# Kernel optimization log

Measured on AMD Instinct MI355X. Metric: run time of the kernel, lower is better.

The kernel has to match this reference:

```python
import jax, jax.numpy as jnp
import numpy as np

N = 50000          # nodes
E = 1_600_000      # edges
IN = 256           # in_channels
C = 32             # hidden_channels (per-head width)
HEADS = 4
BN_EPS = 1e-5


def setup_inputs() -> dict:
    key = jax.random.key(0)
    ks = jax.random.split(key, 32)
    g = lambda k, shp, s=0.1: (jax.random.normal(k, shp, jnp.float32) * s)
    inp = {
        "x": jax.random.normal(ks[0], (N, IN), jnp.float32),
        "edge_index": jax.random.randint(ks[1], (2, E), 0, N, jnp.int64),
        "edge_attr": jax.random.uniform(ks[2], (E, 1), jnp.float32),
        # conv1 (GATConv in=IN, out=C, heads=HEADS, edge_dim=1)
        "W1": g(ks[3], (IN, HEADS * C)),
        "as1": g(ks[4], (HEADS, C)),
        "ad1": g(ks[5], (HEADS, C)),
        "We1": g(ks[6], (1, HEADS * C)),
        "ae1": g(ks[7], (HEADS, C)),
        "b1": jnp.zeros((HEADS * C,), jnp.float32),
        # bn1 (eval mode, running_mean=0, running_var=1)
        "g1": jnp.ones((HEADS * C,), jnp.float32),
        "be1": jnp.zeros((HEADS * C,), jnp.float32),
        # conv2 (GATConv in=HEADS*C, out=C, heads=1, concat=False, edge_dim=1)
        "W2": g(ks[8], (HEADS * C, C)),
        "as2": g(ks[9], (1, C)),
        "ad2": g(ks[10], (1, C)),
        "We2": g(ks[11], (1, C)),
        "ae2": g(ks[12], (1, C)),
        "b2": jnp.zeros((C,), jnp.float32),
        # bn2
        "g2": jnp.ones((C,), jnp.float32),
        "be2": jnp.zeros((C,), jnp.float32),
        # classifier: Linear(C,16) -> ReLU -> Linear(16,2)
        "Wc1": g(ks[13], (C, 16)),
        "bc1": jnp.zeros((16,), jnp.float32),
        "Wc2": g(ks[14], (16, 2)),
        "bc2": jnp.zeros((2,), jnp.float32),
        "Wr1": g(ks[15], (C, 16)),
        "br1": jnp.zeros((16,), jnp.float32),
        "Wr2": g(ks[16], (16, 1)),
        "br2": jnp.zeros((1,), jnp.float32),
    }
    return inp


def _gat_conv(x, src, dst, eattr, W, a_src, a_dst, We, a_e, bias, heads, c, concat):
    n = x.shape[0]
    xs = (x @ W).reshape(n, heads, c)                       # [N,H,C]
    al_s = (xs * a_src).sum(-1)                              # [N,H]
    al_d = (xs * a_dst).sum(-1)                              # [N,H]
    ee = (eattr @ We).reshape(-1, heads, c)                  # [E,H,C]
    al_e = (ee * a_e).sum(-1)                                # [E,H]
    alpha = al_s[src] + al_d[dst] + al_e                     # [E,H]
    alpha = jax.nn.leaky_relu(alpha, 0.2)
    # segment softmax over destination node
    mx = jax.ops.segment_max(alpha, dst, num_segments=n)
    ex = jnp.exp(alpha - mx[dst])
    den = jax.ops.segment_sum(ex, dst, num_segments=n)
    a = ex / (den[dst] + 1e-16)                              # [E,H]
    out = jax.ops.segment_sum(xs[src] * a[..., None], dst, num_segments=n)  # [N,H,C]
    out = out.reshape(n, heads * c) if concat else out.mean(axis=1)
    return out + bias


def _add_self_loops(src, dst, eattr, n):
    loop = jnp.arange(n, dtype=src.dtype)
    fill = jnp.broadcast_to(eattr.mean(axis=0, keepdims=True), (n, eattr.shape[1]))
    return (jnp.concatenate([src, loop]), jnp.concatenate([dst, loop]),
            jnp.concatenate([eattr, fill], axis=0))


def _bn_eval(x, gamma, beta):
    # running_mean=0, running_var=1 (fresh BatchNorm1d, eval mode)
    return x * (gamma / jnp.sqrt(1.0 + BN_EPS)) + beta


def reference(x, edge_index, edge_attr, W1, as1, ad1, We1, ae1, b1, g1, be1,
              W2, as2, ad2, We2, ae2, b2, g2, be2,
              Wc1, bc1, Wc2, bc2, Wr1, br1, Wr2, br2):
    n = x.shape[0]
    src, dst, ea = _add_self_loops(edge_index[0], edge_index[1], edge_attr, n)
    h = _gat_conv(x, src, dst, ea, W1, as1, ad1, We1, ae1, b1, HEADS, C, True)
    h = jax.nn.elu(_bn_eval(h, g1, be1))
    h = _gat_conv(h, src, dst, ea, W2, as2, ad2, We2, ae2, b2, 1, C, False)
    h = jax.nn.elu(_bn_eval(h, g2, be2))
    cls = jax.nn.relu(h @ Wc1 + bc1) @ Wc2 + bc2             # [N,2]
    reg = (jax.nn.relu(h @ Wr1 + br1) @ Wr2 + br2)[:, 0]     # [N]
    return cls, reg, h
```

## Files before the change

kernel.cpp:

```cpp
#include <hip/hip_runtime.h>
#include <cstdint>
#include <cstddef>

#define NN 50000
#define EE 1600000
#define IN_DIM 256
#define HC 128
#define CD 32
#define BN_RS 0.9999950000374997f

#define CAP1 128
#define CAP2 128
#define NBKT 196
#define S1_B 782
#define HIST_B 160
#define G1_B 782

typedef __attribute__((ext_vector_type(8))) short short8;
typedef __attribute__((ext_vector_type(4))) float f32x4;

__device__ __forceinline__ float lrelu(float a) { return a > 0.f ? a : 0.2f * a; }
__device__ __forceinline__ float elu(float a) { return a > 0.f ? a : (__expf(a) - 1.f); }

__device__ __forceinline__ unsigned short f2bf(float f) {
    unsigned int u = __float_as_uint(f);
    unsigned int r = (u + 0x7FFFu + ((u >> 16) & 1u)) >> 16;
    return (unsigned short)r;
}
__device__ __forceinline__ float bf2f(unsigned short b) {
    return __uint_as_float(((unsigned int)b) << 16);
}
__device__ __forceinline__ float2 bf2f2(unsigned int p) {
    float2 r;
    r.x = __uint_as_float(p << 16);
    r.y = __uint_as_float(p & 0xFFFF0000u);
    return r;
}
__device__ __forceinline__ void unpack_edge(unsigned long long p, int& s, float& eav) {
    s = (int)(unsigned int)(p & 0xFFFFFFFFull);
    eav = __uint_as_float((unsigned int)(p >> 32));
}

__device__ __forceinline__ int block_excl_scan_256(int v, int tid, int* wsum) {
    int lane = tid & 63, wv = tid >> 6;
    int x = v;
    #pragma unroll
    for (int off = 1; off < 64; off <<= 1) {
        int y = __shfl_up(x, off);
        if (lane >= off) x += y;
    }
    if (lane == 63) wsum[wv] = x;
    __syncthreads();
    int wpre = 0;
    #pragma unroll
    for (int w = 0; w < 4; w++)
        if (w < wv) wpre += wsum[w];
    return wpre + x - v;
}

__global__ __launch_bounds__(256) void k0_prep(const float* __restrict__ W1,
                                               const float* __restrict__ W2,
                                               const float* __restrict__ We1,
                                               const float* __restrict__ ae1,
                                               const float* __restrict__ We2,
                                               const float* __restrict__ ae2,
                                               unsigned short* __restrict__ W1hi,
                                               unsigned short* __restrict__ W1lo,
                                               unsigned short* __restrict__ W2hi,
                                               unsigned short* __restrict__ W2lo,
                                               float* __restrict__ consts) {
    int blk = blockIdx.x;
    int tid = threadIdx.x;
    if (blk < 16) {
        int t = blk * 256 + tid;
        int lane = t & 63;
        int kt = (t >> 6) & 7;
        int nt = t >> 9;
        int kbase = kt * 32 + (lane >> 4) * 8;
        int col = nt * 16 + (lane & 15);
        size_t obase = (size_t)t * 8;
        #pragma unroll
        for (int j = 0; j < 8; j++) {
            float w = W1[(size_t)(kbase + j) * HC + col];
            unsigned short h = f2bf(w);
            W1hi[obase + j] = h;
            W1lo[obase + j] = f2bf(w - bf2f(h));
        }
    } else if (blk < 18) {
        int t = (blk - 16) * 256 + tid;
        int lane = t & 63;
        int kt = (t >> 6) & 3;
        int nt = t >> 8;
        int kbase = kt * 32 + (lane >> 4) * 8;
        int col = nt * 16 + (lane & 15);
        size_t obase = (size_t)t * 8;
        #pragma unroll
        for (int j = 0; j < 8; j++) {
            float w = W2[(size_t)(kbase + j) * CD + col];
            unsigned short h = f2bf(w);
            W2hi[obase + j] = h;
            W2lo[obase + j] = f2bf(w - bf2f(h));
        }
    } else {
        if (tid < 4) {
            float s = 0.f;
            for (int c = 0; c < 32; c++) s += We1[tid * 32 + c] * ae1[tid * 32 + c];
            consts[2 + tid] = s;
        } else if (tid == 4) {
            float s = 0.f;
            for (int c = 0; c < 32; c++) s += We2[c] * ae2[c];
            consts[6] = s;
        }
    }
}

__global__ __launch_bounds__(256) void kA_hist_gemm1(const int* __restrict__ ei,
                                                     const float* __restrict__ ea,
                                                     const float* __restrict__ x,
                                                     const unsigned short* __restrict__ Whi,
                                                     const unsigned short* __restrict__ Wlo,
                                                     int* __restrict__ bucketHist,
                                                     float* __restrict__ easum,
                                                     unsigned short* __restrict__ xs1b) {
    __shared__ int h[256];
    int tid = threadIdx.x;
    if (blockIdx.x < HIST_B) {
        h[tid] = 0;
        __syncthreads();
        float s = 0.f;
        for (int i = blockIdx.x * 256 + tid; i < EE; i += HIST_B * 256) {
            atomicAdd(&h[ei[EE + i] >> 8], 1);
            s += ea[i];
        }
        __syncthreads();
        if (tid < NBKT && h[tid] > 0) atomicAdd(&bucketHist[tid], h[tid]);
        #pragma unroll
        for (int off = 32; off > 0; off >>= 1) s += __shfl_xor(s, off);
        if ((tid & 63) == 0) atomicAdd(easum, s);
    } else {
        int lane = tid & 63, wv = tid >> 6;
        int row0 = (blockIdx.x - HIST_B) * 64 + wv * 16;
        if (row0 >= NN) return;
        int m = lane & 15;
        int q = lane >> 4;
        f32x4 acc[8];
        #pragma unroll
        for (int nt = 0; nt < 8; nt++) acc[nt] = {0.f, 0.f, 0.f, 0.f};
        const float* xrow = x + (size_t)(row0 + m) * IN_DIM + q * 8;
        #pragma unroll
        for (int kt = 0; kt < 8; kt++) {
            float4 v0 = *(const float4*)(xrow + kt * 32);
            float4 v1 = *(const float4*)(xrow + kt * 32 + 4);
            float vv[8] = {v0.x, v0.y, v0.z, v0.w, v1.x, v1.y, v1.z, v1.w};
            short8 ahi, alo;
            #pragma unroll
            for (int j = 0; j < 8; j++) {
                unsigned short hh = f2bf(vv[j]);
                ahi[j] = (short)hh;
                alo[j] = (short)f2bf(vv[j] - bf2f(hh));
            }
            #pragma unroll
            for (int nt = 0; nt < 8; nt++) {
                size_t fb = ((size_t)(nt * 8 + kt) * 64 + lane) * 8;
                short8 bhi = *(const short8*)(Whi + fb);
                short8 blo = *(const short8*)(Wlo + fb);
                acc[nt] = __builtin_amdgcn_mfma_f32_16x16x32_bf16(ahi, bhi, acc[nt], 0, 0, 0);
                acc[nt] = __builtin_amdgcn_mfma_f32_16x16x32_bf16(ahi, blo, acc[nt], 0, 0, 0);
                acc[nt] = __builtin_amdgcn_mfma_f32_16x16x32_bf16(alo, bhi, acc[nt], 0, 0, 0);
            }
        }
        #pragma unroll
        for (int nt = 0; nt < 8; nt++) {
            #pragma unroll
            for (int reg = 0; reg < 4; reg++) {
                int row = row0 + q * 4 + reg;
                xs1b[(size_t)row * HC + nt * 16 + m] = f2bf(acc[nt][reg]);
            }
        }
    }
}

__global__ void bucket_scan(const int* __restrict__ bucketHist,
                            int* __restrict__ bucketBase,
                            int* __restrict__ bucketCursor,
                            int* __restrict__ indptr,
                            float* __restrict__ consts) {
    __shared__ int wsum[4];
    int tid = threadIdx.x;
    int v = (tid < NBKT) ? bucketHist[tid] : 0;
    int excl = block_excl_scan_256(v, tid, wsum);
    if (tid <= NBKT) bucketBase[tid] = (tid == NBKT) ? EE : excl;
    if (tid < NBKT) bucketCursor[tid] = excl;
    if (tid == 0) { indptr[NN] = EE; consts[1] = consts[0] / (float)EE; }
}

__global__ __launch_bounds__(256) void kB_stage1_al1(const int* __restrict__ ei,
                                                     const float* __restrict__ ea,
                                                     int* __restrict__ bucketCursor,
                                                     int* __restrict__ Adst,
                                                     int* __restrict__ Asrc,
                                                     float* __restrict__ Aea,
                                                     const unsigned short* __restrict__ xs1b,
                                                     const float* __restrict__ as1,
                                                     const float* __restrict__ ad1,
                                                     float* __restrict__ als,
                                                     float* __restrict__ ald) {
    __shared__ int cnt[256];
    __shared__ int basel[256];
    __shared__ int gbase[256];
    __shared__ int wsum[4];
    __shared__ int sdst[2048];
    __shared__ int ssrc[2048];
    __shared__ float sea[2048];
    int tid = threadIdx.x;
    if (blockIdx.x < S1_B) {
        int base = blockIdx.x * 2048;
        cnt[tid] = 0;
        __syncthreads();
        int d[8], s[8], r[8], bk[8];
        float e[8];
        #pragma unroll
        for (int k = 0; k < 8; k++) {
            int i = base + k * 256 + tid;
            if (i < EE) {
                d[k] = ei[EE + i];
                s[k] = ei[i];
                e[k] = ea[i];
                bk[k] = d[k] >> 8;
                r[k] = atomicAdd(&cnt[bk[k]], 1);
            } else d[k] = -1;
        }
        __syncthreads();
        int v = cnt[tid];
        int excl = block_excl_scan_256(v, tid, wsum);
        basel[tid] = excl;
        if (tid < NBKT) gbase[tid] = atomicAdd(&bucketCursor[tid], v);
        __syncthreads();
        #pragma unroll
        for (int k = 0; k < 8; k++) {
            if (d[k] >= 0) {
                int slot = basel[bk[k]] + r[k];
                sdst[slot] = d[k];
                ssrc[slot] = s[k];
                sea[slot] = e[k];
            }
        }
        __syncthreads();
        int total = basel[255] + cnt[255];
        for (int slot = tid; slot < total; slot += 256) {
            int dd = sdst[slot];
            int b = dd >> 8;
            int pos = gbase[b] + (slot - basel[b]);
            Adst[pos] = dd;
            Asrc[pos] = ssrc[slot];
            Aea[pos] = sea[slot];
        }
    } else {
        int t = (blockIdx.x - S1_B) * 256 + tid;
        if (t < NN * 4) {
            int hh = t & 3;
            const unsigned int* xp = (const unsigned int*)(xs1b + (size_t)t * 32);
            const float* ap = as1 + hh * 32;
            const float* dp = ad1 + hh * 32;
            float s = 0.f, d = 0.f;
            #pragma unroll
            for (int q = 0; q < 16; q++) {
                float2 v = bf2f2(xp[q]);
                s += v.x * ap[q * 2] + v.y * ap[q * 2 + 1];
                d += v.x * dp[q * 2] + v.y * dp[q * 2 + 1];
            }
            als[t] = s;
            ald[t] = d;
        }
    }
}

__global__ __launch_bounds__(256) void stage2_kernel(const int* __restrict__ bucketBase,
                                                     const int* __restrict__ Adst,
                                                     const int* __restrict__ Asrc,
                                                     const float* __restrict__ Aea,
                                                     int* __restrict__ indptr,
                                                     unsigned long long* __restrict__ edgedat) {
    __shared__ int cnt[256];
    __shared__ int dbase[256];
    __shared__ int wsum[4];
    int tid = threadIdx.x;
    int b = blockIdx.x;
    int start = bucketBase[b], end = bucketBase[b + 1];
    cnt[tid] = 0;
    __syncthreads();
    for (int i = start + tid; i < end; i += 256) atomicAdd(&cnt[Adst[i] & 255], 1);
    __syncthreads();
    int v = cnt[tid];
    int excl = block_excl_scan_256(v, tid, wsum);
    dbase[tid] = excl;
    __syncthreads();
    int n = b * 256 + tid;
    if (n < NN) indptr[n] = start + excl;
    cnt[tid] = 0;
    __syncthreads();
    for (int i = start + tid; i < end; i += 256) {
        int dl = Adst[i] & 255;
        int r = atomicAdd(&cnt[dl], 1);
        int pos = start + dbase[dl] + r;
        edgedat[pos] = (unsigned long long)(unsigned int)Asrc[i] |
                       ((unsigned long long)__float_as_uint(Aea[i]) << 32);
    }
}

__global__ __launch_bounds__(256) void gat1_agg(
    const unsigned short* __restrict__ xs1b, const float* __restrict__ als,
    const float* __restrict__ ald, const unsigned long long* __restrict__ edgedat,
    const int* __restrict__ indptr, const float* __restrict__ consts,
    const float* __restrict__ b1, const float* __restrict__ g1,
    const float* __restrict__ be1,
    unsigned short* __restrict__ h1hi, unsigned short* __restrict__ h1lo) {
    __shared__ float exbuf[4][CAP1 * 4];
    __shared__ int srcbuf[4][CAP1];
    int wv = threadIdx.x >> 6;
    int lane = threadIdx.x & 63;
    int n = blockIdx.x * 4 + wv;
    int start = indptr[n];
    int deg = indptr[n + 1] - start;
    float ea_mean = consts[1];
    float ce[4] = {consts[2], consts[3], consts[4], consts[5]};
    float4 a4d = *(const float4*)(ald + (size_t)n * 4);
    float aldh[4] = {a4d.x, a4d.y, a4d.z, a4d.w};
    float4 a4s = *(const float4*)(als + (size_t)n * 4);
    float alsn[4] = {a4s.x, a4s.y, a4s.z, a4s.w};
    float ex0[4], sm[4];
    #pragma unroll
    for (int h = 0; h < 4; h++) {
        ex0[h] = __expf(lrelu(alsn[h] + aldh[h] + ea_mean * ce[h]));
        sm[h] = 0.f;
    }
    const unsigned long long* edp = edgedat + start;
    for (int i = lane; i < deg; i += 64) {
        int s; float eav;
        unpack_edge(edp[i], s, eav);
        float4 v4 = *(const float4*)(als + (size_t)s * 4);
        float alv[4] = {v4.x, v4.y, v4.z, v4.w};
        bool st = (i < CAP1);
        if (st) srcbuf[wv][i] = s * HC;
        #pragma unroll
        for (int h = 0; h < 4; h++) {
            float exv = __expf(lrelu(alv[h] + aldh[h] + eav * ce[h]));
            if (st) exbuf[wv][i * 4 + h] = exv;
            sm[h] += exv;
        }
    }
    #pragma unroll
    for (int h = 0; h < 4; h++)
        for (int off = 32; off > 0; off >>= 1) sm[h] += __shfl_xor(sm[h], off);
    float inv[4];
    #pragma unroll
    for (int h = 0; h < 4; h++) inv[h] = 1.0f / (sm[h] + ex0[h] + 1e-16f);
    int mcap = deg < CAP1 ? deg : CAP1;
    for (int i = lane; i < mcap; i += 64) {
        #pragma unroll
        for (int h = 0; h < 4; h++) exbuf[wv][i * 4 + h] *= inv[h];
    }
    int c = lane * 2;
    int h = lane >> 4;
    float wsl = ex0[h] * inv[h];
    float2 vself = bf2f2(*(const unsigned int*)(xs1b + (size_t)n * HC + c));
    float accx = vself.x * wsl, accy = vself.y * wsl;
    int i = 0;
    for (; i + 4 <= mcap; i += 4) {
        float w0 = exbuf[wv][(i + 0) * 4 + h];
        float w1 = exbuf[wv][(i + 1) * 4 + h];
        float w2 = exbuf[wv][(i + 2) * 4 + h];
        float w3 = exbuf[wv][(i + 3) * 4 + h];
        int o0 = srcbuf[wv][i + 0], o1 = srcbuf[wv][i + 1];
        int o2 = srcbuf[wv][i + 2], o3 = srcbuf[wv][i + 3];
        float2 v0 = bf2f2(*(const unsigned int*)(xs1b + o0 + c));
        float2 v1 = bf2f2(*(const unsigned int*)(xs1b + o1 + c));
        float2 v2 = bf2f2(*(const unsigned int*)(xs1b + o2 + c));
        float2 v3 = bf2f2(*(const unsigned int*)(xs1b + o3 + c));
        accx += v0.x * w0; accy += v0.y * w0;
        accx += v1.x * w1; accy += v1.y * w1;
        accx += v2.x * w2; accy += v2.y * w2;
        accx += v3.x * w3; accy += v3.y * w3;
    }
    for (; i < mcap; i++) {
        float w0 = exbuf[wv][i * 4 + h];
        int o0 = srcbuf[wv][i];
        float2 v0 = bf2f2(*(const unsigned int*)(xs1b + o0 + c));
        accx += v0.x * w0; accy += v0.y * w0;
    }
    for (; i < deg; i++) {
        int s; float eav;
        unpack_edge(edp[i], s, eav);
        float a = lrelu(als[(size_t)s * 4 + h] + aldh[h] + eav * ce[h]);
        float w0 = __expf(a) * inv[h];
        float2 v0 = bf2f2(*(const unsigned int*)(xs1b + (size_t)s * HC + c));
        accx += v0.x * w0; accy += v0.y * w0;
    }
    float o0 = accx + b1[c];
    float o1 = accy + b1[c + 1];
    o0 = o0 * (g1[c] * BN_RS) + be1[c];
    o1 = o1 * (g1[c + 1] * BN_RS) + be1[c + 1];
    o0 = elu(o0);
    o1 = elu(o1);
    unsigned short h0 = f2bf(o0), h1v = f2bf(o1);
    unsigned short l0 = f2bf(o0 - bf2f(h0)), l1 = f2bf(o1 - bf2f(h1v));
    *(unsigned int*)(h1hi + (size_t)n * HC + c) = (unsigned int)h0 | ((unsigned int)h1v << 16);
    *(unsigned int*)(h1lo + (size_t)n * HC + c) = (unsigned int)l0 | ((unsigned int)l1 << 16);
}

__global__ __launch_bounds__(256) void gemm2_mfma(const unsigned short* __restrict__ h1hi,
                                                  const unsigned short* __restrict__ h1lo,
                                                  const unsigned short* __restrict__ W2hi,
                                                  const unsigned short* __restrict__ W2lo,
                                                  const float* __restrict__ as2,
                                                  const float* __restrict__ ad2,
                                                  unsigned short* __restrict__ xs2b,
                                                  float* __restrict__ als2,
                                                  float* __restrict__ ald2) {
    int tid = threadIdx.x;
    int lane = tid & 63, wv = tid >> 6;
    int row0 = blockIdx.x * 64 + wv * 16;
    if (row0 >= NN) return;
    int m = lane & 15, q = lane >> 4;
    f32x4 acc[2];
    acc[0] = {0.f, 0.f, 0.f, 0.f};
    acc[1] = {0.f, 0.f, 0.f, 0.f};
    const unsigned short* rhi = h1hi + (size_t)(row0 + m) * HC + q * 8;
    const unsigned short* rlo = h1lo + (size_t)(row0 + m) * HC + q * 8;
    #pragma unroll
    for (int kt = 0; kt < 4; kt++) {
        short8 ahi = *(const short8*)(rhi + kt * 32);
        short8 alo = *(const short8*)(rlo + kt * 32);
        #pragma unroll
        for (int nt = 0; nt < 2; nt++) {
            size_t fb = ((size_t)(nt * 4 + kt) * 64 + lane) * 8;
            short8 bhi = *(const short8*)(W2hi + fb);
            short8 blo = *(const short8*)(W2lo + fb);
            acc[nt] = __builtin_amdgcn_mfma_f32_16x16x32_bf16(ahi, bhi, acc[nt], 0, 0, 0);
            acc[nt] = __builtin_amdgcn_mfma_f32_16x16x32_bf16(ahi, blo, acc[nt], 0, 0, 0);
            acc[nt] = __builtin_amdgcn_mfma_f32_16x16x32_bf16(alo, bhi, acc[nt], 0, 0, 0);
        }
    }
    float a0 = as2[m], a1 = as2[m + 16];
    float d0 = ad2[m], d1 = ad2[m + 16];
    #pragma unroll
    for (int reg = 0; reg < 4; reg++) {
        int row = row0 + q * 4 + reg;
        xs2b[(size_t)row * CD + m]      = f2bf(acc[0][reg]);
        xs2b[(size_t)row * CD + 16 + m] = f2bf(acc[1][reg]);
        float s = acc[0][reg] * a0 + acc[1][reg] * a1;
        float d = acc[0][reg] * d0 + acc[1][reg] * d1;
        #pragma unroll
        for (int off = 1; off < 16; off <<= 1) {
            s += __shfl_xor(s, off);
            d += __shfl_xor(d, off);
        }
        if (m == 0) { als2[row] = s; ald2[row] = d; }
    }
}

__global__ __launch_bounds__(256) void gat2_agg(
    const unsigned short* __restrict__ xs2b, const float* __restrict__ als,
    const float* __restrict__ ald, const unsigned long long* __restrict__ edgedat,
    const int* __restrict__ indptr, const float* __restrict__ consts,
    const float* __restrict__ b2, const float* __restrict__ g2, const float* __restrict__ be2,
    const float* __restrict__ Wc1, const float* __restrict__ bc1,
    const float* __restrict__ Wc2, const float* __restrict__ bc2,
    const float* __restrict__ Wr1, const float* __restrict__ br1,
    const float* __restrict__ Wr2, const float* __restrict__ br2,
    float* __restrict__ hout, float* __restrict__ cls, float* __restrict__ reg) {
    __shared__ float exbuf[4][CAP2];
    __shared__ int srcbuf[4][CAP2];
    __shared__ float hbuf[4][32];
    int wv = threadIdx.x >> 6;
    int lane = threadIdx.x & 63;
    int n = blockIdx.x * 4 + wv;
    int start = indptr[n];
    int deg = indptr[n + 1] - start;
    float ea_mean = consts[1];
    float ce = consts[6];
    float aldn = ald[n];
    float ex0 = __expf(lrelu(als[n] + aldn + ea_mean * ce));
    float sm = 0.f;
    const unsigned long long* edp = edgedat + start;
    for (int i = lane; i < deg; i += 64) {
        int s; float eav;
        unpack_edge(edp[i], s, eav);
        float exv = __expf(lrelu(als[s] + aldn + eav * ce));
        if (i < CAP2) { srcbuf[wv][i] = s * CD; exbuf[wv][i] = exv; }
        sm += exv;
    }
    for (int off = 32; off > 0; off >>= 1) sm += __shfl_xor(sm, off);
    float invd = 1.0f / (sm + ex0 + 1e-16f);
    int mcap = deg < CAP2 ? deg : CAP2;
    for (int i = lane; i < mcap; i += 64) exbuf[wv][i] *= invd;
    int quarter = lane >> 4;
    int cl = lane & 15;
    int c = cl * 2;
    float accx = 0.f, accy = 0.f;
    if (quarter == 0) {
        float2 vs = bf2f2(*(const unsigned int*)(xs2b + (size_t)n * CD + c));
        float wsl = ex0 * invd;
        accx = vs.x * wsl; accy = vs.y * wsl;
    }
    for (int i = quarter; i < mcap; i += 4) {
        float w0 = exbuf[wv][i];
        int o0 = srcbuf[wv][i];
        float2 v0 = bf2f2(*(const unsigned int*)(xs2b + o0 + c));
        accx += v0.x * w0; accy += v0.y * w0;
    }
    for (int i = CAP2 + quarter; i < deg; i += 4) {
        int s; float eav;
        unpack_edge(edp[i], s, eav);
        float w0 = __expf(lrelu(als[s] + aldn + eav * ce)) * invd;
        float2 v0 = bf2f2(*(const unsigned int*)(xs2b + (size_t)s * CD + c));
        accx += v0.x * w0; accy += v0.y * w0;
    }
    accx += __shfl_xor(accx, 16); accy += __shfl_xor(accy, 16);
    accx += __shfl_xor(accx, 32); accy += __shfl_xor(accy, 32);
    if (lane < 16) {
        float o0 = accx + b2[c];
        float o1 = accy + b2[c + 1];
        o0 = o0 * (g2[c] * BN_RS) + be2[c];
        o1 = o1 * (g2[c + 1] * BN_RS) + be2[c + 1];
        o0 = elu(o0);
        o1 = elu(o1);
        hbuf[wv][c] = o0;
        hbuf[wv][c + 1] = o1;
        *(float2*)(hout + (size_t)n * CD + c) = make_float2(o0, o1);
    }
    __syncthreads();
    float r0 = 0.f, r1 = 0.f;
    if (lane < 32) {
        int j = lane & 15;
        bool iscls = lane < 16;
        float s = iscls ? bc1[j] : br1[j];
        #pragma unroll
        for (int cc = 0; cc < 32; cc++) {
            float w = iscls ? Wc1[cc * 16 + j] : Wr1[cc * 16 + j];
            s += hbuf[wv][cc] * w;
        }
        s = fmaxf(s, 0.f);
        if (iscls) { r0 = s * Wc2[j * 2]; r1 = s * Wc2[j * 2 + 1]; }
        else       { r0 = s * Wr2[j]; }
    }
    #pragma unroll
    for (int off = 1; off < 16; off <<= 1) {
        r0 += __shfl_xor(r0, off);
        r1 += __shfl_xor(r1, off);
    }
    if (lane == 0)  *(float2*)(cls + (size_t)n * 2) = make_float2(r0 + bc2[0], r1 + bc2[1]);
    if (lane == 16) reg[n] = r0 + br2[0];
}

extern "C" void kernel_launch(void* const* d_in, const int* in_sizes, int n_in,
                              void* d_out, int out_size, void* d_ws, size_t ws_size,
                              hipStream_t stream) {
    const float* x   = (const float*)d_in[0];
    const int*   ei  = (const int*)d_in[1];
    const float* ea  = (const float*)d_in[2];
    const float* W1  = (const float*)d_in[3];
    const float* as1 = (const float*)d_in[4];
    const float* ad1 = (const float*)d_in[5];
    const float* We1 = (const float*)d_in[6];
    const float* ae1 = (const float*)d_in[7];
    const float* b1  = (const float*)d_in[8];
    const float* g1  = (const float*)d_in[9];
    const float* be1 = (const float*)d_in[10];
    const float* W2  = (const float*)d_in[11];
    const float* as2 = (const float*)d_in[12];
    const float* ad2 = (const float*)d_in[13];
    const float* We2 = (const float*)d_in[14];
    const float* ae2 = (const float*)d_in[15];
    const float* b2  = (const float*)d_in[16];
    const float* g2  = (const float*)d_in[17];
    const float* be2 = (const float*)d_in[18];
    const float* Wc1 = (const float*)d_in[19];
    const float* bc1 = (const float*)d_in[20];
    const float* Wc2 = (const float*)d_in[21];
    const float* bc2 = (const float*)d_in[22];
    const float* Wr1 = (const float*)d_in[23];
    const float* br1 = (const float*)d_in[24];
    const float* Wr2 = (const float*)d_in[25];
    const float* br2 = (const float*)d_in[26];

    char* ws = (char*)d_ws;
    unsigned short* xs1b = (unsigned short*)(ws + 0);
    unsigned short* h1hi = (unsigned short*)(ws + 12800000);
    unsigned short* h1lo = (unsigned short*)(ws + 25600000);
    int*   Adst          = (int*)(ws + 12800000);
    int*   Asrc          = (int*)(ws + 19200000);
    float* Aea           = (float*)(ws + 25600000);
    unsigned short* xs2b = (unsigned short*)(ws + 38400000);
    float* als1          = (float*)(ws + 41600000);
    float* ald1          = (float*)(ws + 42400000);
    float* als2          = (float*)(ws + 43200000);
    float* ald2          = (float*)(ws + 43400000);
    float* consts        = (float*)(ws + 43600000);
    int*   bucketHist    = (int*)(ws + 43600128);
    int*   bucketBase    = (int*)(ws + 43601024);
    int*   bucketCursor  = (int*)(ws + 43601920);
    int*   indptr        = (int*)(ws + 43602816);
    unsigned long long* edgedat = (unsigned long long*)(ws + 43802824);
    unsigned short* W1hi = (unsigned short*)(ws + 56602832);
    unsigned short* W1lo = (unsigned short*)(ws + 56668368);
    unsigned short* W2hi = (unsigned short*)(ws + 56733904);
    unsigned short* W2lo = (unsigned short*)(ws + 56742096);

    float* out_cls = (float*)d_out;
    float* out_reg = out_cls + 2 * NN;
    float* out_h   = out_cls + 3 * NN;

    hipMemsetAsync(bucketHist, 0, NBKT * sizeof(int), stream);
    hipMemsetAsync(consts, 0, 8 * sizeof(float), stream);

    k0_prep<<<19, 256, 0, stream>>>(W1, W2, We1, ae1, We2, ae2,
                                    W1hi, W1lo, W2hi, W2lo, consts);
    kA_hist_gemm1<<<HIST_B + G1_B, 256, 0, stream>>>(ei, ea, x, W1hi, W1lo,
                                                     bucketHist, consts, xs1b);
    bucket_scan<<<1, 256, 0, stream>>>(bucketHist, bucketBase, bucketCursor, indptr, consts);
    kB_stage1_al1<<<S1_B + 782, 256, 0, stream>>>(ei, ea, bucketCursor, Adst, Asrc, Aea,
                                                  xs1b, as1, ad1, als1, ald1);
    stage2_kernel<<<NBKT, 256, 0, stream>>>(bucketBase, Adst, Asrc, Aea, indptr, edgedat);

    gat1_agg<<<NN / 4, 256, 0, stream>>>(xs1b, als1, ald1, edgedat, indptr, consts,
                                         b1, g1, be1, h1hi, h1lo);
    gemm2_mfma<<<G1_B, 256, 0, stream>>>(h1hi, h1lo, W2hi, W2lo, as2, ad2,
                                         xs2b, als2, ald2);
    gat2_agg<<<NN / 4, 256, 0, stream>>>(xs2b, als2, ald2, edgedat, indptr, consts,
                                         b2, g2, be2, Wc1, bc1, Wc2, bc2,
                                         Wr1, br1, Wr2, br2, out_h, out_cls, out_reg);
}
```

Before: 361.4 us.

## Fuse GAT layer-1 aggregation with layer-2 MFMA projection via LDS tile

```diff
diff --git a/kernel.cpp b/kernel.cpp
--- a/kernel.cpp
+++ b/kernel.cpp
@@ -15,6 +15,7 @@
 #define S1_B 782
 #define HIST_B 160
 #define G1_B 782
+#define PADW 136
 
 typedef __attribute__((ext_vector_type(8))) short short8;
 typedef __attribute__((ext_vector_type(4))) float f32x4;
@@ -68,7 +69,8 @@
                                                unsigned short* __restrict__ W1lo,
                                                unsigned short* __restrict__ W2hi,
                                                unsigned short* __restrict__ W2lo,
-                                               float* __restrict__ consts) {
+                                               float* __restrict__ consts,
+                                               int* __restrict__ bucketHist) {
     int blk = blockIdx.x;
     int tid = threadIdx.x;
     if (blk < 16) {
@@ -102,6 +104,8 @@
             W2lo[obase + j] = f2bf(w - bf2f(h));
         }
     } else {
+        if (tid < NBKT) bucketHist[tid] = 0;
+        if (tid == 200) consts[0] = 0.f;
         if (tid < 4) {
             float s = 0.f;
             for (int c = 0; c < 32; c++) s += We1[tid * 32 + c] * ae1[tid * 32 + c];
@@ -308,154 +312,149 @@
     }
 }
 
-__global__ __launch_bounds__(256) void gat1_agg(
+__global__ __launch_bounds__(256) void gat1_fused(
     const unsigned short* __restrict__ xs1b, const float* __restrict__ als,
     const float* __restrict__ ald, const unsigned long long* __restrict__ edgedat,
     const int* __restrict__ indptr, const float* __restrict__ consts,
     const float* __restrict__ b1, const float* __restrict__ g1,
     const float* __restrict__ be1,
-    unsigned short* __restrict__ h1hi, unsigned short* __restrict__ h1lo) {
+    const unsigned short* __restrict__ W2hi, const unsigned short* __restrict__ W2lo,
+    const float* __restrict__ as2, const float* __restrict__ ad2,
+    unsigned short* __restrict__ xs2b, float* __restrict__ als2, float* __restrict__ ald2) {
     __shared__ float exbuf[4][CAP1 * 4];
     __shared__ int srcbuf[4][CAP1];
+    __shared__ unsigned short h1hiL[16][PADW];
+    __shared__ unsigned short h1loL[16][PADW];
+    __shared__ float sred[4][16];
     int wv = threadIdx.x >> 6;
     int lane = threadIdx.x & 63;
-    int n = blockIdx.x * 4 + wv;
-    int start = indptr[n];
-    int deg = indptr[n + 1] - start;
+    int c = lane * 2;
+    int h = lane >> 4;
     float ea_mean = consts[1];
     float ce[4] = {consts[2], consts[3], consts[4], consts[5]};
-    float4 a4d = *(const float4*)(ald + (size_t)n * 4);
-    float aldh[4] = {a4d.x, a4d.y, a4d.z, a4d.w};
-    float4 a4s = *(const float4*)(als + (size_t)n * 4);
-    float alsn[4] = {a4s.x, a4s.y, a4s.z, a4s.w};
-    float ex0[4], sm[4];
-    #pragma unroll
-    for (int h = 0; h < 4; h++) {
-        ex0[h] = __expf(lrelu(alsn[h] + aldh[h] + ea_mean * ce[h]));
-        sm[h] = 0.f;
-    }
-    const unsigned long long* edp = edgedat + start;
-    for (int i = lane; i < deg; i += 64) {
-        int s; float eav;
-        unpack_edge(edp[i], s, eav);
-        float4 v4 = *(const float4*)(als + (size_t)s * 4);
-        float alv[4] = {v4.x, v4.y, v4.z, v4.w};
-        bool st = (i < CAP1);
-        if (st) srcbuf[wv][i] = s * HC;
-        #pragma unroll
-        for (int h = 0; h < 4; h++) {
-            float exv = __expf(lrelu(alv[h] + aldh[h] + eav * ce[h]));
-            if (st) exbuf[wv][i * 4 + h] = exv;
-            sm[h] += exv;
-        }
-    }
-    #pragma unroll
-    for (int h = 0; h < 4; h++)
-        for (int off = 32; off > 0; off >>= 1) sm[h] += __shfl_xor(sm[h], off);
-    float inv[4];
-    #pragma unroll
-    for (int h = 0; h < 4; h++) inv[h] = 1.0f / (sm[h] + ex0[h] + 1e-16f);
-    int mcap = deg < CAP1 ? deg : CAP1;
-    for (int i = lane; i < mcap; i += 64) {
-        #pragma unroll
-        for (int h = 0; h < 4; h++) exbuf[wv][i * 4 + h] *= inv[h];
-    }
-    int c = lane * 2;
-    int h = lane >> 4;
-    float wsl = ex0[h] * inv[h];
-    float2 vself = bf2f2(*(const unsigned int*)(xs1b + (size_t)n * HC + c));
-    float accx = vself.x * wsl, accy = vself.y * wsl;
-    int i = 0;
-    for (; i + 4 <= mcap; i += 4) {
-        float w0 = exbuf[wv][(i + 0) * 4 + h];
-        float w1 = exbuf[wv][(i + 1) * 4 + h];
-        float w2 = exbuf[wv][(i + 2) * 4 + h];
-        float w3 = exbuf[wv][(i + 3) * 4 + h];
-        int o0 = srcbuf[wv][i + 0], o1 = srcbuf[wv][i + 1];
-        int o2 = srcbuf[wv][i + 2], o3 = srcbuf[wv][i + 3];
-        float2 v0 = bf2f2(*(const unsigned int*)(xs1b + o0 + c));
-        float2 v1 = bf2f2(*(const unsigned int*)(xs1b + o1 + c));
-        float2 v2 = bf2f2(*(const unsigned int*)(xs1b + o2 + c));
-        float2 v3 = bf2f2(*(const unsigned int*)(xs1b + o3 + c));
-        accx += v0.x * w0; accy += v0.y * w0;
-        accx += v1.x * w1; accy += v1.y * w1;
-        accx += v2.x * w2; accy += v2.y * w2;
-        accx += v3.x * w3; accy += v3.y * w3;
-    }
-    for (; i < mcap; i++) {
-        float w0 = exbuf[wv][i * 4 + h];
-        int o0 = srcbuf[wv][i];
-        float2 v0 = bf2f2(*(const unsigned int*)(xs1b + o0 + c));
-        accx += v0.x * w0; accy += v0.y * w0;
-    }
-    for (; i < deg; i++) {
-        int s; float eav;
-        unpack_edge(edp[i], s, eav);
-        float a = lrelu(als[(size_t)s * 4 + h] + aldh[h] + eav * ce[h]);
-        float w0 = __expf(a) * inv[h];
-        float2 v0 = bf2f2(*(const unsigned int*)(xs1b + (size_t)s * HC + c));
-        accx += v0.x * w0; accy += v0.y * w0;
-    }
-    float o0 = accx + b1[c];
-    float o1 = accy + b1[c + 1];
-    o0 = o0 * (g1[c] * BN_RS) + be1[c];
-    o1 = o1 * (g1[c + 1] * BN_RS) + be1[c + 1];
-    o0 = elu(o0);
-    o1 = elu(o1);
-    unsigned short h0 = f2bf(o0), h1v = f2bf(o1);
-    unsigned short l0 = f2bf(o0 - bf2f(h0)), l1 = f2bf(o1 - bf2f(h1v));
-    *(unsigned int*)(h1hi + (size_t)n * HC + c) = (unsigned int)h0 | ((unsigned int)h1v << 16);
-    *(unsigned int*)(h1lo + (size_t)n * HC + c) = (unsigned int)l0 | ((unsigned int)l1 << 16);
-}
-
-__global__ __launch_bounds__(256) void gemm2_mfma(const unsigned short* __restrict__ h1hi,
-                                                  const unsigned short* __restrict__ h1lo,
-                                                  const unsigned short* __restrict__ W2hi,
-                                                  const unsigned short* __restrict__ W2lo,
-                                                  const float* __restrict__ as2,
-                                                  const float* __restrict__ ad2,
-                                                  unsigned short* __restrict__ xs2b,
-                                                  float* __restrict__ als2,
-                                                  float* __restrict__ ald2) {
-    int tid = threadIdx.x;
-    int lane = tid & 63, wv = tid >> 6;
-    int row0 = blockIdx.x * 64 + wv * 16;
-    if (row0 >= NN) return;
-    int m = lane & 15, q = lane >> 4;
-    f32x4 acc[2];
-    acc[0] = {0.f, 0.f, 0.f, 0.f};
-    acc[1] = {0.f, 0.f, 0.f, 0.f};
-    const unsigned short* rhi = h1hi + (size_t)(row0 + m) * HC + q * 8;
-    const unsigned short* rlo = h1lo + (size_t)(row0 + m) * HC + q * 8;
-    #pragma unroll
-    for (int kt = 0; kt < 4; kt++) {
-        short8 ahi = *(const short8*)(rhi + kt * 32);
-        short8 alo = *(const short8*)(rlo + kt * 32);
-        #pragma unroll
-        for (int nt = 0; nt < 2; nt++) {
-            size_t fb = ((size_t)(nt * 4 + kt) * 64 + lane) * 8;
+    for (int t = 0; t < 4; t++) {
+        int n = blockIdx.x * 16 + wv * 4 + t;
+        int start = indptr[n];
+        int deg = indptr[n + 1] - start;
+        float4 a4d = *(const float4*)(ald + (size_t)n * 4);
+        float aldh[4] = {a4d.x, a4d.y, a4d.z, a4d.w};
+        float4 a4s = *(const float4*)(als + (size_t)n * 4);
+        float alsn[4] = {a4s.x, a4s.y, a4s.z, a4s.w};
+        float ex0[4], sm[4];
+        #pragma unroll
+        for (int hh = 0; hh < 4; hh++) {
+            ex0[hh] = __expf(lrelu(alsn[hh] + aldh[hh] + ea_mean * ce[hh]));
+            sm[hh] = 0.f;
+        }
+        const unsigned long long* edp = edgedat + start;
+        for (int i = lane; i < deg; i += 64) {
+            int s; float eav;
+            unpack_edge(edp[i], s, eav);
+            float4 v4 = *(const float4*)(als + (size_t)s * 4);
+            float alv[4] = {v4.x, v4.y, v4.z, v4.w};
+            bool st = (i < CAP1);
+            if (st) srcbuf[wv][i] = s * HC;
+            #pragma unroll
+            for (int hh = 0; hh < 4; hh++) {
+                float exv = __expf(lrelu(alv[hh] + aldh[hh] + eav * ce[hh]));
+                if (st) exbuf[wv][i * 4 + hh] = exv;
+                sm[hh] += exv;
+            }
+        }
+        #pragma unroll
+        for (int hh = 0; hh < 4; hh++)
+            for (int off = 32; off > 0; off >>= 1) sm[hh] += __shfl_xor(sm[hh], off);
+        float inv[4];
+        #pragma unroll
+        for (int hh = 0; hh < 4; hh++) inv[hh] = 1.0f / (sm[hh] + ex0[hh] + 1e-16f);
+        int mcap = deg < CAP1 ? deg : CAP1;
+        for (int i = lane; i < mcap; i += 64) {
+            #pragma unroll
+            for (int hh = 0; hh < 4; hh++) exbuf[wv][i * 4 + hh] *= inv[hh];
+        }
+        float wsl = ex0[h] * inv[h];
+        float2 vself = bf2f2(*(const unsigned int*)(xs1b + (size_t)n * HC + c));
+        float accx = vself.x * wsl, accy = vself.y * wsl;
+        int i = 0;
+        for (; i + 4 <= mcap; i += 4) {
+            float w0 = exbuf[wv][(i + 0) * 4 + h];
+            float w1 = exbuf[wv][(i + 1) * 4 + h];
+            float w2 = exbuf[wv][(i + 2) * 4 + h];
+            float w3 = exbuf[wv][(i + 3) * 4 + h];
+            int o0 = srcbuf[wv][i + 0], o1 = srcbuf[wv][i + 1];
+            int o2 = srcbuf[wv][i + 2], o3 = srcbuf[wv][i + 3];
+            float2 v0 = bf2f2(*(const unsigned int*)(xs1b + o0 + c));
+            float2 v1 = bf2f2(*(const unsigned int*)(xs1b + o1 + c));
+            float2 v2 = bf2f2(*(const unsigned int*)(xs1b + o2 + c));
+            float2 v3 = bf2f2(*(const unsigned int*)(xs1b + o3 + c));
+            accx += v0.x * w0; accy += v0.y * w0;
+            accx += v1.x * w1; accy += v1.y * w1;
+            accx += v2.x * w2; accy += v2.y * w2;
+            accx += v3.x * w3; accy += v3.y * w3;
+        }
+        for (; i < mcap; i++) {
+            float w0 = exbuf[wv][i * 4 + h];
+            int o0 = srcbuf[wv][i];
+            float2 v0 = bf2f2(*(const unsigned int*)(xs1b + o0 + c));
+            accx += v0.x * w0; accy += v0.y * w0;
+        }
+        for (; i < deg; i++) {
+            int s; float eav;
+            unpack_edge(edp[i], s, eav);
+            float a = lrelu(als[(size_t)s * 4 + h] + aldh[h] + eav * ce[h]);
+            float w0 = __expf(a) * inv[h];
+            float2 v0 = bf2f2(*(const unsigned int*)(xs1b + (size_t)s * HC + c));
+            accx += v0.x * w0; accy += v0.y * w0;
+        }
+        float o0 = accx + b1[c];
+        float o1 = accy + b1[c + 1];
+        o0 = o0 * (g1[c] * BN_RS) + be1[c];
+        o1 = o1 * (g1[c + 1] * BN_RS) + be1[c + 1];
+        o0 = elu(o0);
+        o1 = elu(o1);
+        int lrow = wv * 4 + t;
+        unsigned short h0 = f2bf(o0), h1v = f2bf(o1);
+        unsigned short l0 = f2bf(o0 - bf2f(h0)), l1 = f2bf(o1 - bf2f(h1v));
+        *(unsigned int*)&h1hiL[lrow][c] = (unsigned int)h0 | ((unsigned int)h1v << 16);
+        *(unsigned int*)&h1loL[lrow][c] = (unsigned int)l0 | ((unsigned int)l1 << 16);
+    }
+    __syncthreads();
+    if (wv < 2) {
+        int m = lane & 15, q = lane >> 4;
+        f32x4 acc = {0.f, 0.f, 0.f, 0.f};
+        #pragma unroll
+        for (int kt = 0; kt < 4; kt++) {
+            short8 ahi = *(const short8*)&h1hiL[m][kt * 32 + q * 8];
+            short8 alo = *(const short8*)&h1loL[m][kt * 32 + q * 8];
+            size_t fb = ((size_t)(wv * 4 + kt) * 64 + lane) * 8;
             short8 bhi = *(const short8*)(W2hi + fb);
             short8 blo = *(const short8*)(W2lo + fb);
-            acc[nt] = __builtin_amdgcn_mfma_f32_16x16x32_bf16(ahi, bhi, acc[nt], 0, 0, 0);
-            acc[nt] = __builtin_amdgcn_mfma_f32_16x16x32_bf16(ahi, blo, acc[nt], 0, 0, 0);
-            acc[nt] = __builtin_amdgcn_mfma_f32_16x16x32_bf16(alo, bhi, acc[nt], 0, 0, 0);
-        }
-    }
-    float a0 = as2[m], a1 = as2[m + 16];
-    float d0 = ad2[m], d1 = ad2[m + 16];
-    #pragma unroll
-    for (int reg = 0; reg < 4; reg++) {
-        int row = row0 + q * 4 + reg;
-        xs2b[(size_t)row * CD + m]      = f2bf(acc[0][reg]);
-        xs2b[(size_t)row * CD + 16 + m] = f2bf(acc[1][reg]);
-        float s = acc[0][reg] * a0 + acc[1][reg] * a1;
-        float d = acc[0][reg] * d0 + acc[1][reg] * d1;
-        #pragma unroll
-        for (int off = 1; off < 16; off <<= 1) {
-            s += __shfl_xor(s, off);
-            d += __shfl_xor(d, off);
-        }
-        if (m == 0) { als2[row] = s; ald2[row] = d; }
+            acc = __builtin_amdgcn_mfma_f32_16x16x32_bf16(ahi, bhi, acc, 0, 0, 0);
+            acc = __builtin_amdgcn_mfma_f32_16x16x32_bf16(ahi, blo, acc, 0, 0, 0);
+            acc = __builtin_amdgcn_mfma_f32_16x16x32_bf16(alo, bhi, acc, 0, 0, 0);
+        }
+        float a0 = as2[wv * 16 + m];
+        float d0 = ad2[wv * 16 + m];
+        #pragma unroll
+        for (int reg = 0; reg < 4; reg++) {
+            int lrow = q * 4 + reg;
+            int row = blockIdx.x * 16 + lrow;
+            xs2b[(size_t)row * CD + wv * 16 + m] = f2bf(acc[reg]);
+            float s = acc[reg] * a0;
+            float d = acc[reg] * d0;
+            #pragma unroll
+            for (int off = 1; off < 16; off <<= 1) {
+                s += __shfl_xor(s, off);
+                d += __shfl_xor(d, off);
+            }
+            if (m == 0) { sred[wv * 2 + 0][lrow] = s; sred[wv * 2 + 1][lrow] = d; }
+        }
+    }
+    __syncthreads();
+    if (threadIdx.x < 16) {
+        int row = blockIdx.x * 16 + threadIdx.x;
+        als2[row] = sred[0][threadIdx.x] + sred[2][threadIdx.x];
+        ald2[row] = sred[1][threadIdx.x] + sred[3][threadIdx.x];
     }
 }
 
@@ -586,8 +585,6 @@
 
     char* ws = (char*)d_ws;
     unsigned short* xs1b = (unsigned short*)(ws + 0);
-    unsigned short* h1hi = (unsigned short*)(ws + 12800000);
-    unsigned short* h1lo = (unsigned short*)(ws + 25600000);
     int*   Adst          = (int*)(ws + 12800000);
     int*   Asrc          = (int*)(ws + 19200000);
     float* Aea           = (float*)(ws + 25600000);
@@ -611,11 +608,8 @@
     float* out_reg = out_cls + 2 * NN;
     float* out_h   = out_cls + 3 * NN;
 
-    hipMemsetAsync(bucketHist, 0, NBKT * sizeof(int), stream);
-    hipMemsetAsync(consts, 0, 8 * sizeof(float), stream);
-
     k0_prep<<<19, 256, 0, stream>>>(W1, W2, We1, ae1, We2, ae2,
-                                    W1hi, W1lo, W2hi, W2lo, consts);
+                                    W1hi, W1lo, W2hi, W2lo, consts, bucketHist);
     kA_hist_gemm1<<<HIST_B + G1_B, 256, 0, stream>>>(ei, ea, x, W1hi, W1lo,
                                                      bucketHist, consts, xs1b);
     bucket_scan<<<1, 256, 0, stream>>>(bucketHist, bucketBase, bucketCursor, indptr, consts);
@@ -623,10 +617,9 @@
                                                   xs1b, as1, ad1, als1, ald1);
     stage2_kernel<<<NBKT, 256, 0, stream>>>(bucketBase, Adst, Asrc, Aea, indptr, edgedat);
 
-    gat1_agg<<<NN / 4, 256, 0, stream>>>(xs1b, als1, ald1, edgedat, indptr, consts,
-                                         b1, g1, be1, h1hi, h1lo);
-    gemm2_mfma<<<G1_B, 256, 0, stream>>>(h1hi, h1lo, W2hi, W2lo, as2, ad2,
-                                         xs2b, als2, ald2);
+    gat1_fused<<<NN / 16, 256, 0, stream>>>(xs1b, als1, ald1, edgedat, indptr, consts,
+                                            b1, g1, be1, W2hi, W2lo, as2, ad2,
+                                            xs2b, als2, ald2);
     gat2_agg<<<NN / 4, 256, 0, stream>>>(xs2b, als2, ald2, edgedat, indptr, consts,
                                          b2, g2, be2, Wc1, bc1, Wc2, bc2,
                                          Wr1, br1, Wr2, br2, out_h, out_cls, out_reg);
```

New measurement: 368.7 us. 1.02x slower.

## Fold memsets into prep kernel, widen stage2 blocks, double histogram blocks

Applied to the files above, without the earlier changes.

```diff
diff --git a/kernel.cpp b/kernel.cpp
--- a/kernel.cpp
+++ b/kernel.cpp
@@ -13,7 +13,7 @@
 #define CAP2 128
 #define NBKT 196
 #define S1_B 782
-#define HIST_B 160
+#define HIST_B 320
 #define G1_B 782
 
 typedef __attribute__((ext_vector_type(8))) short short8;
@@ -68,7 +68,8 @@
                                                unsigned short* __restrict__ W1lo,
                                                unsigned short* __restrict__ W2hi,
                                                unsigned short* __restrict__ W2lo,
-                                               float* __restrict__ consts) {
+                                               float* __restrict__ consts,
+                                               int* __restrict__ bucketHist) {
     int blk = blockIdx.x;
     int tid = threadIdx.x;
     if (blk < 16) {
@@ -102,6 +103,8 @@
             W2lo[obase + j] = f2bf(w - bf2f(h));
         }
     } else {
+        if (tid < NBKT) bucketHist[tid] = 0;
+        if (tid == 200) consts[0] = 0.f;
         if (tid < 4) {
             float s = 0.f;
             for (int c = 0; c < 32; c++) s += We1[tid * 32 + c] * ae1[tid * 32 + c];
@@ -275,31 +278,45 @@
     }
 }
 
-__global__ __launch_bounds__(256) void stage2_kernel(const int* __restrict__ bucketBase,
-                                                     const int* __restrict__ Adst,
-                                                     const int* __restrict__ Asrc,
-                                                     const float* __restrict__ Aea,
-                                                     int* __restrict__ indptr,
-                                                     unsigned long long* __restrict__ edgedat) {
+__global__ __launch_bounds__(1024) void stage2_kernel(const int* __restrict__ bucketBase,
+                                                      const int* __restrict__ Adst,
+                                                      const int* __restrict__ Asrc,
+                                                      const float* __restrict__ Aea,
+                                                      int* __restrict__ indptr,
+                                                      unsigned long long* __restrict__ edgedat) {
     __shared__ int cnt[256];
     __shared__ int dbase[256];
-    __shared__ int wsum[4];
     int tid = threadIdx.x;
     int b = blockIdx.x;
     int start = bucketBase[b], end = bucketBase[b + 1];
-    cnt[tid] = 0;
+    if (tid < 256) cnt[tid] = 0;
     __syncthreads();
-    for (int i = start + tid; i < end; i += 256) atomicAdd(&cnt[Adst[i] & 255], 1);
+    for (int i = start + tid; i < end; i += 1024) atomicAdd(&cnt[Adst[i] & 255], 1);
     __syncthreads();
-    int v = cnt[tid];
-    int excl = block_excl_scan_256(v, tid, wsum);
-    dbase[tid] = excl;
+    if (tid < 64) {
+        int b4 = tid * 4;
+        int c0 = cnt[b4], c1 = cnt[b4 + 1], c2 = cnt[b4 + 2], c3 = cnt[b4 + 3];
+        int t = c0 + c1 + c2 + c3;
+        int x = t;
+        #pragma unroll
+        for (int off = 1; off < 64; off <<= 1) {
+            int y = __shfl_up(x, off);
+            if (tid >= off) x += y;
+        }
+        int e0 = x - t;
+        dbase[b4] = e0;
+        dbase[b4 + 1] = e0 + c0;
+        dbase[b4 + 2] = e0 + c0 + c1;
+        dbase[b4 + 3] = e0 + c0 + c1 + c2;
+    }
     __syncthreads();
-    int n = b * 256 + tid;
-    if (n < NN) indptr[n] = start + excl;
-    cnt[tid] = 0;
+    if (tid < 256) {
+        int n = b * 256 + tid;
+        if (n < NN) indptr[n] = start + dbase[tid];
+        cnt[tid] = 0;
+    }
     __syncthreads();
-    for (int i = start + tid; i < end; i += 256) {
+    for (int i = start + tid; i < end; i += 1024) {
         int dl = Adst[i] & 255;
         int r = atomicAdd(&cnt[dl], 1);
         int pos = start + dbase[dl] + r;
@@ -611,17 +628,14 @@
     float* out_reg = out_cls + 2 * NN;
     float* out_h   = out_cls + 3 * NN;
 
-    hipMemsetAsync(bucketHist, 0, NBKT * sizeof(int), stream);
-    hipMemsetAsync(consts, 0, 8 * sizeof(float), stream);
-
     k0_prep<<<19, 256, 0, stream>>>(W1, W2, We1, ae1, We2, ae2,
-                                    W1hi, W1lo, W2hi, W2lo, consts);
+                                    W1hi, W1lo, W2hi, W2lo, consts, bucketHist);
     kA_hist_gemm1<<<HIST_B + G1_B, 256, 0, stream>>>(ei, ea, x, W1hi, W1lo,
                                                      bucketHist, consts, xs1b);
     bucket_scan<<<1, 256, 0, stream>>>(bucketHist, bucketBase, bucketCursor, indptr, consts);
     kB_stage1_al1<<<S1_B + 782, 256, 0, stream>>>(ei, ea, bucketCursor, Adst, Asrc, Aea,
                                                   xs1b, as1, ad1, als1, ald1);
-    stage2_kernel<<<NBKT, 256, 0, stream>>>(bucketBase, Adst, Asrc, Aea, indptr, edgedat);
+    stage2_kernel<<<NBKT, 1024, 0, stream>>>(bucketBase, Adst, Asrc, Aea, indptr, edgedat);
 
     gat1_agg<<<NN / 4, 256, 0, stream>>>(xs1b, als1, ald1, edgedat, indptr, consts,
                                          b1, g1, be1, h1hi, h1lo);
```

Result: faster. 353.7 us (-2.1%).
